# Performance work log

Hardware: AMD Instinct MI355X
Metric: run time of the kernel (lower is better)

Reference implementation:

```python
import jax, jax.numpy as jnp
import numpy as np

N = 50000   # nodes
E = 800000  # edges (avg degree 16)
D = 128     # emb_dim
K = 3       # message passing rounds


def setup_inputs() -> dict:
    key = jax.random.key(0)
    ks = jax.random.split(key, 24)
    scale = jnp.float32(0.1)  # keep k iterated MLP magnitudes sane

    def w(k, shape):
        return jax.random.normal(k, shape, dtype=jnp.float32) * scale

    inp = {
        "feat": jax.random.normal(ks[0], (N, D), dtype=jnp.float32),
        "src": jax.random.randint(ks[1], (E,), 0, N, dtype=jnp.int32),
        "dst": jax.random.randint(ks[2], (E,), 0, N, dtype=jnp.int32),
    }
    i = 3
    for name in ["nt", "fp", "fu", "bp", "bu"]:
        inp[name + "_w1"] = w(ks[i], (D, D))
        inp[name + "_b1"] = w(ks[i + 1], (D,))
        inp[name + "_w2"] = w(ks[i + 2], (D, D))
        inp[name + "_b2"] = w(ks[i + 3], (D,))
        i += 4
    return inp


def _fnn(x, w1, b1, w2, b2):
    # FNN(in,[hid],out): Linear -> ReLU -> Linear (no final activation)
    return jnp.maximum(x @ w1 + b1, 0.0) @ w2 + b2


def _aggregate(y, src, dst, pw1, pb1, pw2, pb2, uw1, ub1, uw2, ub2):
    # gather src node states -> edge MLP (+ReLU) -> scatter-sum -> node MLP (+ReLU)
    msg = jnp.maximum(_fnn(y[src], pw1, pb1, pw2, pb2), 0.0)   # [E, D]
    z = jax.ops.segment_sum(msg, dst, num_segments=N)          # [N, D]
    return jnp.maximum(_fnn(z, uw1, ub1, uw2, ub2), 0.0)       # [N, D]


def _message_pass(self_trans, src, dst, sink, params):
    y = self_trans
    for _ in range(K):
        h = _aggregate(y, src, dst, *params)
        h = h.at[sink].set(0.0)  # zero the sink node row
        y = self_trans + h
    return y


def reference(feat, src, dst,
              nt_w1, nt_b1, nt_w2, nt_b2,
              fp_w1, fp_b1, fp_w2, fp_b2,
              fu_w1, fu_b1, fu_w2, fu_b2,
              bp_w1, bp_b1, bp_w2, bp_b2,
              bu_w1, bu_b1, bu_w2, bu_b2):
    self_trans = _fnn(feat, nt_w1, nt_b1, nt_w2, nt_b2)  # [N, D]
    # forward-direction aggregator, sink = last node
    out_fpa = _message_pass(self_trans, src, dst, N - 1,
                            (fp_w1, fp_b1, fp_w2, fp_b2,
                             fu_w1, fu_b1, fu_w2, fu_b2))
    # reversed graph (dgl.reverse swaps src/dst), sink = node 0
    out_bpa = _message_pass(self_trans, dst, src, 0,
                            (bp_w1, bp_b1, bp_w2, bp_b2,
                             bu_w1, bu_b1, bu_w2, bu_b2))
    return jnp.concatenate([out_fpa, out_bpa], axis=1)  # [N, 2D]
```

## Files before the change

kernel.cpp:

```cpp
#include <hip/hip_runtime.h>

#define Nn 50000
#define Ee 800000
#define Dd 128
#define Kk 3
#define TEA 32
#define NT 256

#define LSTR 136
#define WSLOT 32768

#define NBUK 196
#define SCH 2048
#define SB ((Ee + SCH - 1) / SCH)
#define FCAP 5632

typedef short sh8 __attribute__((ext_vector_type(8)));
typedef float f32x4 __attribute__((ext_vector_type(4)));

__device__ __forceinline__ ushort bfsplit(float x, float* rem) {
  const unsigned u = __float_as_uint(x);
  *rem = x - __uint_as_float(u & 0xffff0000u);
  return (ushort)(u >> 16);
}
__device__ __forceinline__ ushort bftrunc(float x) {
  return (ushort)(__float_as_uint(x) >> 16);
}
__device__ __forceinline__ ushort f32_to_bf16_rtn(float x) {
  const unsigned u = __float_as_uint(x);
  return (ushort)((u + 0x7fffu + ((u >> 16) & 1u)) >> 16);
}

__device__ __forceinline__ void acc8(const uint4 v, float4& a0, float4& a1) {
  a0.x += __uint_as_float(v.x << 16);
  a0.y += __uint_as_float(v.x & 0xffff0000u);
  a0.z += __uint_as_float(v.y << 16);
  a0.w += __uint_as_float(v.y & 0xffff0000u);
  a1.x += __uint_as_float(v.z << 16);
  a1.y += __uint_as_float(v.z & 0xffff0000u);
  a1.z += __uint_as_float(v.w << 16);
  a1.w += __uint_as_float(v.w & 0xffff0000u);
}

#define MFMA_LAYER(WH, WL, MT)                                                 \
  {                                                                            \
    _Pragma("unroll")                                                          \
    for (int c = 0; c < 4; ++c) {                                              \
      const sh8 bh0 = *(const sh8*)((WH) + (((nt0    ) * 4 + c) * 64 + lane) * 8); \
      const sh8 bh1 = *(const sh8*)((WH) + (((nt0 + 1) * 4 + c) * 64 + lane) * 8); \
      const sh8 bl0 = *(const sh8*)((WL) + (((nt0    ) * 4 + c) * 64 + lane) * 8); \
      const sh8 bl1 = *(const sh8*)((WL) + (((nt0 + 1) * 4 + c) * 64 + lane) * 8); \
      _Pragma("unroll")                                                        \
      for (int mt = 0; mt < (MT); ++mt) {                                      \
        const int aoff = (mt * 16 + l15) * LSTR + c * 32 + q8 * 8;             \
        const sh8 ah = *(const sh8*)(Sh + aoff);                               \
        const sh8 al = *(const sh8*)(Sl + aoff);                               \
        acc[mt][0] = __builtin_amdgcn_mfma_f32_16x16x32_bf16(ah, bh0, acc[mt][0], 0, 0, 0); \
        acc[mt][1] = __builtin_amdgcn_mfma_f32_16x16x32_bf16(ah, bh1, acc[mt][1], 0, 0, 0); \
        acc[mt][0] = __builtin_amdgcn_mfma_f32_16x16x32_bf16(al, bh0, acc[mt][0], 0, 0, 0); \
        acc[mt][1] = __builtin_amdgcn_mfma_f32_16x16x32_bf16(al, bh1, acc[mt][1], 0, 0, 0); \
        acc[mt][0] = __builtin_amdgcn_mfma_f32_16x16x32_bf16(ah, bl0, acc[mt][0], 0, 0, 0); \
        acc[mt][1] = __builtin_amdgcn_mfma_f32_16x16x32_bf16(ah, bl1, acc[mt][1], 0, 0, 0); \
      }                                                                        \
    }                                                                          \
  }

#define ZERO_ACC(MT)                                             \
  {                                                              \
    _Pragma("unroll")                                            \
    for (int mt = 0; mt < (MT); ++mt)                            \
      _Pragma("unroll")                                          \
      for (int nl = 0; nl < 2; ++nl) {                           \
        acc[mt][nl][0] = 0.f; acc[mt][nl][1] = 0.f;              \
        acc[mt][nl][2] = 0.f; acc[mt][nl][3] = 0.f;              \
      }                                                          \
  }

#define HIDDEN_TO_LDS(B1ptr, MT)                                 \
  {                                                              \
    const float b1a = (B1ptr)[w32 + l15];                        \
    const float b1b = (B1ptr)[w32 + 16 + l15];                   \
    _Pragma("unroll")                                            \
    for (int mt = 0; mt < (MT); ++mt)                            \
      _Pragma("unroll")                                          \
      for (int nl = 0; nl < 2; ++nl) {                           \
        const int col = w32 + nl * 16 + l15;                     \
        const float bb = nl ? b1b : b1a;                         \
        _Pragma("unroll")                                        \
        for (int rg = 0; rg < 4; ++rg) {                         \
          const int row = mt * 16 + q8 * 4 + rg;                 \
          const float h = fmaxf(acc[mt][nl][rg] + bb, 0.f);      \
          float rm;                                              \
          const ushort hh = bfsplit(h, &rm);                     \
          const int off = row * LSTR + col;                      \
          Sh[off] = hh;                                          \
          Sl[off] = bftrunc(rm);                                 \
        }                                                        \
      }                                                          \
  }

#define STC_TO_LDS(MT)                                           \
  {                                                              \
    _Pragma("unroll")                                            \
    for (int mt = 0; mt < (MT); ++mt)                            \
      _Pragma("unroll")                                          \
      for (int nl = 0; nl < 2; ++nl) {                           \
        const int col = w32 + nl * 16 + l15;                     \
        _Pragma("unroll")                                        \
        for (int rg = 0; rg < 4; ++rg) {                         \
          const int row = mt * 16 + q8 * 4 + rg;                 \
          float rm;                                              \
          const ushort hh = bfsplit(stc[mt][nl][rg], &rm);       \
          const int off = row * LSTR + col;                      \
          Sh[off] = hh;                                          \
          Sl[off] = bftrunc(rm);                                 \
        }                                                        \
      }                                                          \
  }

#define STAGE_ROWS(Xptr)                                                       \
  {                                                                            \
    _Pragma("unroll")                                                          \
    for (int it = 0; it < (TEA * 32 / NT); ++it) {                             \
      const int i = t + NT * it;                                               \
      const int r = i >> 5;                                                    \
      const int c4 = (i & 31) << 2;                                            \
      float4 v = make_float4(0.f, 0.f, 0.f, 0.f);                              \
      if (r < nrow) v = *(const float4*)((Xptr) + (size_t)(row0 + r) * Dd + c4); \
      ushort4 hv, lv; float rm;                                                \
      hv.x = bfsplit(v.x, &rm); lv.x = bftrunc(rm);                            \
      hv.y = bfsplit(v.y, &rm); lv.y = bftrunc(rm);                            \
      hv.z = bfsplit(v.z, &rm); lv.z = bftrunc(rm);                            \
      hv.w = bfsplit(v.w, &rm); lv.w = bftrunc(rm);                            \
      *(ushort4*)(&Sh[r * LSTR + c4]) = hv;                                    \
      *(ushort4*)(&Sl[r * LSTR + c4]) = lv;                                    \
    }                                                                          \
  }

#define MFMA_PRELUDE(MT)                                         \
  const int lane = t & 63;                                       \
  const int wave = t >> 6;                                       \
  const int l15 = lane & 15;                                     \
  const int q8 = lane >> 4;                                      \
  const int w32 = wave * 32;                                     \
  const int nt0 = wave * 2;                                      \
  f32x4 acc[MT][2];

struct DirP {
  const ushort *u1, *u2, *p1, *p2;
  const float *ub1, *ub2, *pb1, *pb2;
};

__global__ __launch_bounds__(NT) void stmsg_kernel(
    const float* __restrict__ X,
    const ushort* __restrict__ Wn1, const ushort* __restrict__ Wn2,
    const float* __restrict__ Bn1, const float* __restrict__ Bn2,
    DirP pf, DirP pb,
    float* __restrict__ st, ushort* __restrict__ Mf, ushort* __restrict__ Mb)
{
  __shared__ __align__(16) ushort Sbuf[2 * TEA * LSTR];
  ushort* Sh = Sbuf;
  ushort* Sl = Sbuf + TEA * LSTR;
  const int t = threadIdx.x;
  const int row0 = blockIdx.x * TEA;
  const int rem = Nn - row0;
  const int nrow = rem < TEA ? rem : TEA;

  STAGE_ROWS(X);
  __syncthreads();
  MFMA_PRELUDE(2);

  ZERO_ACC(2);
  MFMA_LAYER(Wn1, Wn1 + 16384, 2);
  __syncthreads();
  HIDDEN_TO_LDS(Bn1, 2);
  __syncthreads();
  ZERO_ACC(2);
  MFMA_LAYER(Wn2, Wn2 + 16384, 2);

  float stc[2][2][4];
  {
    const float b2a = Bn2[w32 + l15];
    const float b2b = Bn2[w32 + 16 + l15];
    #pragma unroll
    for (int mt = 0; mt < 2; ++mt)
      #pragma unroll
      for (int nl = 0; nl < 2; ++nl) {
        const int col = w32 + nl * 16 + l15;
        const float bb = nl ? b2b : b2a;
        #pragma unroll
        for (int rg = 0; rg < 4; ++rg) {
          const int row = mt * 16 + q8 * 4 + rg;
          const float v = acc[mt][nl][rg] + bb;
          stc[mt][nl][rg] = v;
          if (row < nrow) st[(size_t)(row0 + row) * Dd + col] = v;
        }
      }
  }
  __syncthreads();

  STC_TO_LDS(2);
  __syncthreads();
  ZERO_ACC(2);
  MFMA_LAYER(pf.p1, pf.p1 + 16384, 2);
  __syncthreads();
  HIDDEN_TO_LDS(pf.pb1, 2);
  __syncthreads();
  ZERO_ACC(2);
  MFMA_LAYER(pf.p2, pf.p2 + 16384, 2);
  {
    const float b2a = pf.pb2[w32 + l15];
    const float b2b = pf.pb2[w32 + 16 + l15];
    #pragma unroll
    for (int mt = 0; mt < 2; ++mt)
      #pragma unroll
      for (int nl = 0; nl < 2; ++nl) {
        const int col = w32 + nl * 16 + l15;
        const float bb = nl ? b2b : b2a;
        #pragma unroll
        for (int rg = 0; rg < 4; ++rg) {
          const int row = mt * 16 + q8 * 4 + rg;
          if (row < nrow)
            Mf[(size_t)(row0 + row) * Dd + col] =
                f32_to_bf16_rtn(fmaxf(acc[mt][nl][rg] + bb, 0.f));
        }
      }
  }
  __syncthreads();

  STC_TO_LDS(2);
  __syncthreads();
  ZERO_ACC(2);
  MFMA_LAYER(pb.p1, pb.p1 + 16384, 2);
  __syncthreads();
  HIDDEN_TO_LDS(pb.pb1, 2);
  __syncthreads();
  ZERO_ACC(2);
  MFMA_LAYER(pb.p2, pb.p2 + 16384, 2);
  {
    const float b2a = pb.pb2[w32 + l15];
    const float b2b = pb.pb2[w32 + 16 + l15];
    #pragma unroll
    for (int mt = 0; mt < 2; ++mt)
      #pragma unroll
      for (int nl = 0; nl < 2; ++nl) {
        const int col = w32 + nl * 16 + l15;
        const float bb = nl ? b2b : b2a;
        #pragma unroll
        for (int rg = 0; rg < 4; ++rg) {
          const int row = mt * 16 + q8 * 4 + rg;
          if (row < nrow)
            Mb[(size_t)(row0 + row) * Dd + col] =
                f32_to_bf16_rtn(fmaxf(acc[mt][nl][rg] + bb, 0.f));
        }
      }
  }
}

template <int DO_MSG>
__global__ __launch_bounds__(NT) void aggupdmsg_kernel(
    const ushort* __restrict__ Min_f, const ushort* __restrict__ Min_b,
    const int* __restrict__ rp_f, const int* __restrict__ rp_b,
    const int* __restrict__ col_f, const int* __restrict__ col_b,
    const float* __restrict__ st,
    ushort* __restrict__ RMf, ushort* __restrict__ RMb,
    float* __restrict__ RYf, float* __restrict__ RYb, int rstride,
    DirP pf, DirP pb, int nhalf)
{
  __shared__ __align__(16) ushort Sbuf[2 * TEA * LSTR];
  ushort* Sh = Sbuf;
  ushort* Sl = Sbuf + TEA * LSTR;
  const int t = threadIdx.x;
  const int dir = blockIdx.x >= nhalf;
  const int row0 = (blockIdx.x - dir * nhalf) * TEA;
  const int rem = Nn - row0;
  const int nrow = rem < TEA ? rem : TEA;
  const DirP P = dir ? pb : pf;
  const ushort* Min = dir ? Min_b : Min_f;
  const int* rp = dir ? rp_b : rp_f;
  const int* col = dir ? col_b : col_f;
  ushort* RoutM = dir ? RMb : RMf;
  float* RoutY = dir ? RYb : RYf;
  const int sink = dir ? 0 : (Nn - 1);

  {
    const int nr = t >> 3;
    const int o8 = t & 7;
    float4 za[4];
    #pragma unroll
    for (int i = 0; i < 4; ++i) za[i] = make_float4(0.f, 0.f, 0.f, 0.f);
    if (nr < nrow) {
      const int gnode = row0 + nr;
      int e = rp[gnode];
      const int ee = rp[gnode + 1];
      const ushort* Mo = Min + o8 * 16;
      for (; e + 3 < ee; e += 4) {
        const int c0 = col[e];
        const int c1 = col[e + 1];
        const int c2 = col[e + 2];
        const int c3 = col[e + 3];
        const ushort* r0 = Mo + (size_t)c0 * Dd;
        const ushort* r1 = Mo + (size_t)c1 * Dd;
        const ushort* r2 = Mo + (size_t)c2 * Dd;
        const ushort* r3 = Mo + (size_t)c3 * Dd;
        uint4 a0 = *(const uint4*)(r0), b0 = *(const uint4*)(r0 + 8);
        uint4 a1 = *(const uint4*)(r1), b1 = *(const uint4*)(r1 + 8);
        uint4 a2 = *(const uint4*)(r2), b2 = *(const uint4*)(r2 + 8);
        uint4 a3 = *(const uint4*)(r3), b3 = *(const uint4*)(r3 + 8);
        acc8(a0, za[0], za[1]); acc8(b0, za[2], za[3]);
        acc8(a1, za[0], za[1]); acc8(b1, za[2], za[3]);
        acc8(a2, za[0], za[1]); acc8(b2, za[2], za[3]);
        acc8(a3, za[0], za[1]); acc8(b3, za[2], za[3]);
      }
      for (; e < ee; ++e) {
        const ushort* r0 = Mo + (size_t)col[e] * Dd;
        acc8(*(const uint4*)(r0), za[0], za[1]);
        acc8(*(const uint4*)(r0 + 8), za[2], za[3]);
      }
    }
    #pragma unroll
    for (int k = 0; k < 4; ++k) {
      ushort4 hv, lv; float rm;
      hv.x = bfsplit(za[k].x, &rm); lv.x = bftrunc(rm);
      hv.y = bfsplit(za[k].y, &rm); lv.y = bftrunc(rm);
      hv.z = bfsplit(za[k].z, &rm); lv.z = bftrunc(rm);
      hv.w = bfsplit(za[k].w, &rm); lv.w = bftrunc(rm);
      const int c4 = o8 * 16 + k * 4;
      *(ushort4*)(&Sh[nr * LSTR + c4]) = hv;
      *(ushort4*)(&Sl[nr * LSTR + c4]) = lv;
    }
  }
  __syncthreads();

  MFMA_PRELUDE(2);

  ZERO_ACC(2);
  MFMA_LAYER(P.u1, P.u1 + 16384, 2);
  __syncthreads();
  HIDDEN_TO_LDS(P.ub1, 2);
  __syncthreads();
  ZERO_ACC(2);
  MFMA_LAYER(P.u2, P.u2 + 16384, 2);

  {
    const float b2a = P.ub2[w32 + l15];
    const float b2b = P.ub2[w32 + 16 + l15];
    if (DO_MSG) __syncthreads();
    #pragma unroll
    for (int mt = 0; mt < 2; ++mt)
      #pragma unroll
      for (int nl = 0; nl < 2; ++nl) {
        const int col = w32 + nl * 16 + l15;
        const float bb = nl ? b2b : b2a;
        #pragma unroll
        for (int rg = 0; rg < 4; ++rg) {
          const int row = mt * 16 + q8 * 4 + rg;
          float v = 0.f;
          if (row < nrow) {
            const int gr = row0 + row;
            v = fmaxf(acc[mt][nl][rg] + bb, 0.f);
            if (gr == sink) v = 0.f;
            v += st[(size_t)gr * Dd + col];
          }
          if (DO_MSG) {
            float rm;
            const ushort hh = bfsplit(v, &rm);
            const int off = row * LSTR + col;
            Sh[off] = hh;
            Sl[off] = bftrunc(rm);
          } else if (row < nrow) {
            RoutY[(size_t)(row0 + row) * rstride + col] = v;
          }
        }
      }
  }

  if (DO_MSG) {
    __syncthreads();
    ZERO_ACC(2);
    MFMA_LAYER(P.p1, P.p1 + 16384, 2);
    __syncthreads();
    HIDDEN_TO_LDS(P.pb1, 2);
    __syncthreads();
    ZERO_ACC(2);
    MFMA_LAYER(P.p2, P.p2 + 16384, 2);

    const float b2a = P.pb2[w32 + l15];
    const float b2b = P.pb2[w32 + 16 + l15];
    #pragma unroll
    for (int mt = 0; mt < 2; ++mt)
      #pragma unroll
      for (int nl = 0; nl < 2; ++nl) {
        const int col = w32 + nl * 16 + l15;
        const float bb = nl ? b2b : b2a;
        #pragma unroll
        for (int rg = 0; rg < 4; ++rg) {
          const int row = mt * 16 + q8 * 4 + rg;
          if (row < nrow)
            RoutM[(size_t)(row0 + row) * Dd + col] =
                f32_to_bf16_rtn(fmaxf(acc[mt][nl][rg] + bb, 0.f));
        }
      }
  }
}

struct WPtrs { const float* w[10]; };

__global__ __launch_bounds__(256) void csr_count(
    const int* __restrict__ src, const int* __restrict__ dst,
    int* __restrict__ bcnt)
{
  const int dirv = blockIdx.y;
  const int* key = dirv ? src : dst;
  __shared__ int h[NBUK];
  const int t = threadIdx.x;
  if (t < NBUK) h[t] = 0;
  __syncthreads();
  const int e0 = blockIdx.x * SCH;
  #pragma unroll
  for (int i = 0; i < SCH / 256; ++i) {
    const int e = e0 + i * 256 + t;
    if (e < Ee) atomicAdd(&h[key[e] >> 8], 1);
  }
  __syncthreads();
  if (t < NBUK && h[t] > 0) atomicAdd(&bcnt[dirv * 256 + t], h[t]);
}

__global__ __launch_bounds__(256) void csr_scan_pack(
    const int* __restrict__ bcnt, int* __restrict__ bbase,
    int* __restrict__ bcur, int* __restrict__ rp,
    WPtrs P, ushort* __restrict__ out)
{
  const int t = threadIdx.x;
  if (blockIdx.x == 0) {
    __shared__ int s[256];
    for (int y = 0; y < 2; ++y) {
      const int v = (t < NBUK) ? bcnt[y * 256 + t] : 0;
      s[t] = v;
      __syncthreads();
      for (int off = 1; off < 256; off <<= 1) {
        int x = s[t];
        if (t >= off) x += s[t - off];
        __syncthreads();
        s[t] = x;
        __syncthreads();
      }
      const int excl = s[t] - v;
      if (t < NBUK) { bbase[y * 257 + t] = excl; bcur[y * 256 + t] = excl; }
      if (t == NBUK - 1) bbase[y * 257 + NBUK] = s[t];
      if (t == 0) rp[y * (Nn + 1) + Nn] = Ee;
      __syncthreads();
    }
  } else {
    const int work = (blockIdx.x - 1) * 256 + t;
    const int mat = work >> 14;
    const int id = work & 16383;
    const int j = id & 7;
    const int lane = (id >> 3) & 63;
    const int ch = (id >> 9) & 3;
    const int nt = id >> 11;
    const int k = ch * 32 + (lane >> 4) * 8 + j;
    const int n = nt * 16 + (lane & 15);
    const float x = P.w[mat][k * Dd + n];
    float rm;
    const ushort h = bfsplit(x, &rm);
    out[(size_t)mat * WSLOT + id] = h;
    out[(size_t)mat * WSLOT + 16384 + id] = bftrunc(rm);
  }
}

__global__ __launch_bounds__(256) void csr_scatter(
    const int* __restrict__ src, const int* __restrict__ dst,
    int* __restrict__ bcur, uint* __restrict__ pairs)
{
  const int dirv = blockIdx.y;
  const int* key = dirv ? src : dst;
  const int* val = dirv ? dst : src;
  __shared__ int lh[NBUK], gb[NBUK], lc[NBUK];
  const int t = threadIdx.x;
  if (t < NBUK) { lh[t] = 0; lc[t] = 0; }
  __syncthreads();
  const int e0 = blockIdx.x * SCH;
  int ks[SCH / 256], vs[SCH / 256];
  #pragma unroll
  for (int i = 0; i < SCH / 256; ++i) {
    const int e = e0 + i * 256 + t;
    ks[i] = (e < Ee) ? key[e] : -1;
    vs[i] = (e < Ee) ? val[e] : 0;
    if (ks[i] >= 0) atomicAdd(&lh[ks[i] >> 8], 1);
  }
  __syncthreads();
  if (t < NBUK && lh[t] > 0) gb[t] = atomicAdd(&bcur[dirv * 256 + t], lh[t]);
  __syncthreads();
  uint* pd = pairs + (size_t)dirv * Ee;
  #pragma unroll
  for (int i = 0; i < SCH / 256; ++i) {
    if (ks[i] >= 0) {
      const int b = ks[i] >> 8;
      const int r = atomicAdd(&lc[b], 1);
      pd[gb[b] + r] = ((uint)ks[i] << 16) | (uint)vs[i];
    }
  }
}

__global__ __launch_bounds__(256) void csr_final(
    const uint* __restrict__ pairs, const int* __restrict__ bbase,
    int* __restrict__ rp, int* __restrict__ col_f, int* __restrict__ col_b)
{
  const int dirv = blockIdx.y;
  const int b = blockIdx.x;
  const int base = bbase[dirv * 257 + b];
  const int cnt = bbase[dirv * 257 + b + 1] - base;
  const uint* pd = pairs + (size_t)dirv * Ee + base;
  int* colo = dirv ? col_b : col_f;
  __shared__ int h[256];
  __shared__ int s[256];
  __shared__ uint pr[FCAP];
  const int t = threadIdx.x;
  h[t] = 0;
  __syncthreads();
  const bool fits = (cnt <= FCAP);
  if (fits) {
    for (int i = t; i < cnt; i += 256) {
      const uint p = pd[i];
      pr[i] = p;
      atomicAdd(&h[(p >> 16) & 255], 1);
    }
  } else {
    for (int i = t; i < cnt; i += 256) atomicAdd(&h[(pd[i] >> 16) & 255], 1);
  }
  __syncthreads();
  const int v = h[t];
  s[t] = v;
  __syncthreads();
  for (int off = 1; off < 256; off <<= 1) {
    int x = s[t];
    if (t >= off) x += s[t - off];
    __syncthreads();
    s[t] = x;
    __syncthreads();
  }
  const int excl = s[t] - v;
  const int node = b * 256 + t;
  if (node < Nn) rp[dirv * (Nn + 1) + node] = base + excl;
  h[t] = excl;
  __syncthreads();
  if (fits) {
    for (int band = 0; band < 8; ++band) {
      for (int i = t; i < cnt; i += 256) {
        const uint p = pr[i];
        const int vv = (int)(p & 0xffffu);
        if ((vv >> 13) == band) {
          const int k = (p >> 16) & 255;
          const int r = atomicAdd(&h[k], 1);
          colo[base + r] = vv;
        }
      }
      __syncthreads();
    }
  } else {
    for (int i = t; i < cnt; i += 256) {
      const uint p = pd[i];
      const int k = (p >> 16) & 255;
      const int r = atomicAdd(&h[k], 1);
      colo[base + r] = (int)(p & 0xffffu);
    }
  }
}

extern "C" void kernel_launch(void* const* d_in, const int* in_sizes, int n_in,
                              void* d_out, int out_size, void* d_ws, size_t ws_size,
                              hipStream_t stream)
{
  const float* feat = (const float*)d_in[0];
  const int*   src  = (const int*)d_in[1];
  const int*   dst  = (const int*)d_in[2];

  const float* W[5][4];
  for (int p = 0; p < 5; ++p)
    for (int q = 0; q < 4; ++q)
      W[p][q] = (const float*)d_in[3 + p * 4 + q];

  float* st = (float*)d_ws;
  ushort* Mp_f = (ushort*)(st + (size_t)Nn * Dd);
  ushort* Mp_b = Mp_f + (size_t)Nn * Dd;
  ushort* Mq_f = Mp_b + (size_t)Nn * Dd;
  ushort* Mq_b = Mq_f + (size_t)Nn * Dd;
  int* ip       = (int*)(Mq_b + (size_t)Nn * Dd);
  int* rp_f     = ip;                 ip += Nn + 1;
  int* rp_b     = ip;                 ip += Nn + 1;
  int* col_f    = ip;                 ip += Ee;
  int* col_b    = ip;                 ip += Ee;
  int* bcnt     = ip;                 ip += 2 * 256;
  int* bbase    = ip;                 ip += 2 * 257;
  int* bcur     = ip;                 ip += 2 * 256;
  ushort* Wp = (ushort*)(((uintptr_t)ip + 63) & ~(uintptr_t)63);
  float* out = (float*)d_out;

  uint* pairs = (uint*)Mq_f;

  const int aggBlocks  = (Nn + TEA - 1) / TEA;
  const int dualBlocks = 2 * aggBlocks;

  WPtrs wpk;
  for (int p = 0; p < 5; ++p) { wpk.w[2 * p] = W[p][0]; wpk.w[2 * p + 1] = W[p][2]; }

  hipMemsetAsync(bcnt, 0, 2 * 256 * sizeof(int), stream);
  csr_count<<<dim3(SB, 2), 256, 0, stream>>>(src, dst, bcnt);
  csr_scan_pack<<<641, 256, 0, stream>>>(bcnt, bbase, bcur, rp_f, wpk, Wp);
  csr_scatter<<<dim3(SB, 2), 256, 0, stream>>>(src, dst, bcur, pairs);
  csr_final<<<dim3(NBUK, 2), 256, 0, stream>>>(pairs, bbase, rp_f, col_f, col_b);

  #define WS(m) (Wp + (size_t)(m) * WSLOT)
  DirP Pf = { WS(4), WS(5), WS(2), WS(3), W[2][1], W[2][3], W[1][1], W[1][3] };
  DirP Pb = { WS(8), WS(9), WS(6), WS(7), W[4][1], W[4][3], W[3][1], W[3][3] };

  stmsg_kernel<<<aggBlocks, NT, 0, stream>>>(
      feat, WS(0), WS(1), W[0][1], W[0][3], Pf, Pb, st, Mp_f, Mp_b);

  aggupdmsg_kernel<1><<<dualBlocks, NT, 0, stream>>>(
      Mp_f, Mp_b, rp_f, rp_b, col_f, col_b, st,
      Mq_f, Mq_b, nullptr, nullptr, 0, Pf, Pb, aggBlocks);

  aggupdmsg_kernel<1><<<dualBlocks, NT, 0, stream>>>(
      Mq_f, Mq_b, rp_f, rp_b, col_f, col_b, st,
      Mp_f, Mp_b, nullptr, nullptr, 0, Pf, Pb, aggBlocks);

  aggupdmsg_kernel<0><<<dualBlocks, NT, 0, stream>>>(
      Mp_f, Mp_b, rp_f, rp_b, col_f, col_b, st,
      nullptr, nullptr, out, out + Dd, 2 * Dd, Pf, Pb, aggBlocks);

  #undef WS
}
```

Baseline: 525.2 us.

## Fuse CSR scatter blocks into self-transform/message kernel grid

Merges the edge scatter pass and the initial node/message MLP kernel into one launch. The first blocks of the grid do the bucket scatter and the rest do the MLP rows. This removes a kernel launch and its serialization, so the memory-bound scatter can overlap with the compute-bound MLP. The MLP blocks now share the grid with scatter blocks that have a different resource profile.

```diff
diff --git a/kernel.cpp b/kernel.cpp
--- a/kernel.cpp
+++ b/kernel.cpp
@@ -151,18 +151,122 @@
   const float *ub1, *ub2, *pb1, *pb2;
 };
 
-__global__ __launch_bounds__(NT) void stmsg_kernel(
+struct WPtrs { const float* w[10]; };
+
+__global__ __launch_bounds__(256) void csr_count(
+    const int* __restrict__ src, const int* __restrict__ dst,
+    int* __restrict__ bcnt)
+{
+  const int dirv = blockIdx.y;
+  const int* key = dirv ? src : dst;
+  __shared__ int h[NBUK];
+  const int t = threadIdx.x;
+  if (t < NBUK) h[t] = 0;
+  __syncthreads();
+  const int e0 = blockIdx.x * SCH;
+  #pragma unroll
+  for (int i = 0; i < SCH / 256; ++i) {
+    const int e = e0 + i * 256 + t;
+    if (e < Ee) atomicAdd(&h[key[e] >> 8], 1);
+  }
+  __syncthreads();
+  if (t < NBUK && h[t] > 0) atomicAdd(&bcnt[dirv * 256 + t], h[t]);
+}
+
+__global__ __launch_bounds__(256) void csr_scan_pack(
+    const int* __restrict__ bcnt, int* __restrict__ bbase,
+    int* __restrict__ bcur, int* __restrict__ rp,
+    WPtrs P, ushort* __restrict__ out)
+{
+  const int t = threadIdx.x;
+  if (blockIdx.x == 0) {
+    __shared__ int s[256];
+    for (int y = 0; y < 2; ++y) {
+      const int v = (t < NBUK) ? bcnt[y * 256 + t] : 0;
+      s[t] = v;
+      __syncthreads();
+      for (int off = 1; off < 256; off <<= 1) {
+        int x = s[t];
+        if (t >= off) x += s[t - off];
+        __syncthreads();
+        s[t] = x;
+        __syncthreads();
+      }
+      const int excl = s[t] - v;
+      if (t < NBUK) { bbase[y * 257 + t] = excl; bcur[y * 256 + t] = excl; }
+      if (t == NBUK - 1) bbase[y * 257 + NBUK] = s[t];
+      if (t == 0) rp[y * (Nn + 1) + Nn] = Ee;
+      __syncthreads();
+    }
+  } else {
+    const int work = (blockIdx.x - 1) * 256 + t;
+    const int mat = work >> 14;
+    const int id = work & 16383;
+    const int j = id & 7;
+    const int lane = (id >> 3) & 63;
+    const int ch = (id >> 9) & 3;
+    const int nt = id >> 11;
+    const int k = ch * 32 + (lane >> 4) * 8 + j;
+    const int n = nt * 16 + (lane & 15);
+    const float x = P.w[mat][k * Dd + n];
+    float rm;
+    const ushort h = bfsplit(x, &rm);
+    out[(size_t)mat * WSLOT + id] = h;
+    out[(size_t)mat * WSLOT + 16384 + id] = bftrunc(rm);
+  }
+}
+
+__global__ __launch_bounds__(NT) void scatter_stmsg_kernel(
+    const int* __restrict__ src, const int* __restrict__ dst,
+    int* __restrict__ bcur, uint* __restrict__ pairs,
     const float* __restrict__ X,
     const ushort* __restrict__ Wn1, const ushort* __restrict__ Wn2,
     const float* __restrict__ Bn1, const float* __restrict__ Bn2,
     DirP pf, DirP pb,
-    float* __restrict__ st, ushort* __restrict__ Mf, ushort* __restrict__ Mb)
+    float* __restrict__ st, ushort* __restrict__ Mf, ushort* __restrict__ Mb,
+    int nScatter)
 {
   __shared__ __align__(16) ushort Sbuf[2 * TEA * LSTR];
+  const int t = threadIdx.x;
+
+  if ((int)blockIdx.x < nScatter) {
+    int* lh = (int*)Sbuf;
+    int* gb = lh + 256;
+    int* lc = gb + 256;
+    const int dirv = (int)blockIdx.x >= SB;
+    const int sb = blockIdx.x - dirv * SB;
+    const int* key = dirv ? src : dst;
+    const int* val = dirv ? dst : src;
+    if (t < NBUK) { lh[t] = 0; lc[t] = 0; }
+    __syncthreads();
+    const int e0 = sb * SCH;
+    int ks[SCH / 256], vs[SCH / 256];
+    #pragma unroll
+    for (int i = 0; i < SCH / 256; ++i) {
+      const int e = e0 + i * 256 + t;
+      ks[i] = (e < Ee) ? key[e] : -1;
+      vs[i] = (e < Ee) ? val[e] : 0;
+      if (ks[i] >= 0) atomicAdd(&lh[ks[i] >> 8], 1);
+    }
+    __syncthreads();
+    if (t < NBUK && lh[t] > 0) gb[t] = atomicAdd(&bcur[dirv * 256 + t], lh[t]);
+    __syncthreads();
+    uint* pd = pairs + (size_t)dirv * Ee;
+    #pragma unroll
+    for (int i = 0; i < SCH / 256; ++i) {
+      if (ks[i] >= 0) {
+        const int b = ks[i] >> 8;
+        const int r = atomicAdd(&lc[b], 1);
+        pd[gb[b] + r] = ((uint)ks[i] << 16) | (uint)vs[i];
+      }
+    }
+    return;
+  }
+
   ushort* Sh = Sbuf;
   ushort* Sl = Sbuf + TEA * LSTR;
-  const int t = threadIdx.x;
-  const int row0 = blockIdx.x * TEA;
+  const int bid = blockIdx.x - nScatter;
+  const int row0 = bid * TEA;
   const int rem = Nn - row0;
   const int nrow = rem < TEA ? rem : TEA;
 
@@ -254,6 +358,71 @@
                 f32_to_bf16_rtn(fmaxf(acc[mt][nl][rg] + bb, 0.f));
         }
       }
+  }
+}
+
+__global__ __launch_bounds__(256) void csr_final(
+    const uint* __restrict__ pairs, const int* __restrict__ bbase,
+    int* __restrict__ rp, int* __restrict__ col_f, int* __restrict__ col_b)
+{
+  const int dirv = blockIdx.y;
+  const int b = blockIdx.x;
+  const int base = bbase[dirv * 257 + b];
+  const int cnt = bbase[dirv * 257 + b + 1] - base;
+  const uint* pd = pairs + (size_t)dirv * Ee + base;
+  int* colo = dirv ? col_b : col_f;
+  __shared__ int h[256];
+  __shared__ int s[256];
+  __shared__ uint pr[FCAP];
+  const int t = threadIdx.x;
+  h[t] = 0;
+  __syncthreads();
+  const bool fits = (cnt <= FCAP);
+  if (fits) {
+    for (int i = t; i < cnt; i += 256) {
+      const uint p = pd[i];
+      pr[i] = p;
+      atomicAdd(&h[(p >> 16) & 255], 1);
+    }
+  } else {
+    for (int i = t; i < cnt; i += 256) atomicAdd(&h[(pd[i] >> 16) & 255], 1);
+  }
+  __syncthreads();
+  const int v = h[t];
+  s[t] = v;
+  __syncthreads();
+  for (int off = 1; off < 256; off <<= 1) {
+    int x = s[t];
+    if (t >= off) x += s[t - off];
+    __syncthreads();
+    s[t] = x;
+    __syncthreads();
+  }
+  const int excl = s[t] - v;
+  const int node = b * 256 + t;
+  if (node < Nn) rp[dirv * (Nn + 1) + node] = base + excl;
+  h[t] = excl;
+  __syncthreads();
+  if (fits) {
+    for (int band = 0; band < 8; ++band) {
+      for (int i = t; i < cnt; i += 256) {
+        const uint p = pr[i];
+        const int vv = (int)(p & 0xffffu);
+        if ((vv >> 13) == band) {
+          const int k = (p >> 16) & 255;
+          const int r = atomicAdd(&h[k], 1);
+          colo[base + r] = vv;
+        }
+      }
+      __syncthreads();
+    }
+  } else {
+    for (int i = t; i < cnt; i += 256) {
+      const uint p = pd[i];
+      const int k = (p >> 16) & 255;
+      const int r = atomicAdd(&h[k], 1);
+      colo[base + r] = (int)(p & 0xffffu);
+    }
   }
 }
 
@@ -404,170 +573,6 @@
   }
 }
 
-struct WPtrs { const float* w[10]; };
-
-__global__ __launch_bounds__(256) void csr_count(
-    const int* __restrict__ src, const int* __restrict__ dst,
-    int* __restrict__ bcnt)
-{
-  const int dirv = blockIdx.y;
-  const int* key = dirv ? src : dst;
-  __shared__ int h[NBUK];
-  const int t = threadIdx.x;
-  if (t < NBUK) h[t] = 0;
-  __syncthreads();
-  const int e0 = blockIdx.x * SCH;
-  #pragma unroll
-  for (int i = 0; i < SCH / 256; ++i) {
-    const int e = e0 + i * 256 + t;
-    if (e < Ee) atomicAdd(&h[key[e] >> 8], 1);
-  }
-  __syncthreads();
-  if (t < NBUK && h[t] > 0) atomicAdd(&bcnt[dirv * 256 + t], h[t]);
-}
-
-__global__ __launch_bounds__(256) void csr_scan_pack(
-    const int* __restrict__ bcnt, int* __restrict__ bbase,
-    int* __restrict__ bcur, int* __restrict__ rp,
-    WPtrs P, ushort* __restrict__ out)
-{
-  const int t = threadIdx.x;
-  if (blockIdx.x == 0) {
-    __shared__ int s[256];
-    for (int y = 0; y < 2; ++y) {
-      const int v = (t < NBUK) ? bcnt[y * 256 + t] : 0;
-      s[t] = v;
-      __syncthreads();
-      for (int off = 1; off < 256; off <<= 1) {
-        int x = s[t];
-        if (t >= off) x += s[t - off];
-        __syncthreads();
-        s[t] = x;
-        __syncthreads();
-      }
-      const int excl = s[t] - v;
-      if (t < NBUK) { bbase[y * 257 + t] = excl; bcur[y * 256 + t] = excl; }
-      if (t == NBUK - 1) bbase[y * 257 + NBUK] = s[t];
-      if (t == 0) rp[y * (Nn + 1) + Nn] = Ee;
-      __syncthreads();
-    }
-  } else {
-    const int work = (blockIdx.x - 1) * 256 + t;
-    const int mat = work >> 14;
-    const int id = work & 16383;
-    const int j = id & 7;
-    const int lane = (id >> 3) & 63;
-    const int ch = (id >> 9) & 3;
-    const int nt = id >> 11;
-    const int k = ch * 32 + (lane >> 4) * 8 + j;
-    const int n = nt * 16 + (lane & 15);
-    const float x = P.w[mat][k * Dd + n];
-    float rm;
-    const ushort h = bfsplit(x, &rm);
-    out[(size_t)mat * WSLOT + id] = h;
-    out[(size_t)mat * WSLOT + 16384 + id] = bftrunc(rm);
-  }
-}
-
-__global__ __launch_bounds__(256) void csr_scatter(
-    const int* __restrict__ src, const int* __restrict__ dst,
-    int* __restrict__ bcur, uint* __restrict__ pairs)
-{
-  const int dirv = blockIdx.y;
-  const int* key = dirv ? src : dst;
-  const int* val = dirv ? dst : src;
-  __shared__ int lh[NBUK], gb[NBUK], lc[NBUK];
-  const int t = threadIdx.x;
-  if (t < NBUK) { lh[t] = 0; lc[t] = 0; }
-  __syncthreads();
-  const int e0 = blockIdx.x * SCH;
-  int ks[SCH / 256], vs[SCH / 256];
-  #pragma unroll
-  for (int i = 0; i < SCH / 256; ++i) {
-    const int e = e0 + i * 256 + t;
-    ks[i] = (e < Ee) ? key[e] : -1;
-    vs[i] = (e < Ee) ? val[e] : 0;
-    if (ks[i] >= 0) atomicAdd(&lh[ks[i] >> 8], 1);
-  }
-  __syncthreads();
-  if (t < NBUK && lh[t] > 0) gb[t] = atomicAdd(&bcur[dirv * 256 + t], lh[t]);
-  __syncthreads();
-  uint* pd = pairs + (size_t)dirv * Ee;
-  #pragma unroll
-  for (int i = 0; i < SCH / 256; ++i) {
-    if (ks[i] >= 0) {
-      const int b = ks[i] >> 8;
-      const int r = atomicAdd(&lc[b], 1);
-      pd[gb[b] + r] = ((uint)ks[i] << 16) | (uint)vs[i];
-    }
-  }
-}
-
-__global__ __launch_bounds__(256) void csr_final(
-    const uint* __restrict__ pairs, const int* __restrict__ bbase,
-    int* __restrict__ rp, int* __restrict__ col_f, int* __restrict__ col_b)
-{
-  const int dirv = blockIdx.y;
-  const int b = blockIdx.x;
-  const int base = bbase[dirv * 257 + b];
-  const int cnt = bbase[dirv * 257 + b + 1] - base;
-  const uint* pd = pairs + (size_t)dirv * Ee + base;
-  int* colo = dirv ? col_b : col_f;
-  __shared__ int h[256];
-  __shared__ int s[256];
-  __shared__ uint pr[FCAP];
-  const int t = threadIdx.x;
-  h[t] = 0;
-  __syncthreads();
-  const bool fits = (cnt <= FCAP);
-  if (fits) {
-    for (int i = t; i < cnt; i += 256) {
-      const uint p = pd[i];
-      pr[i] = p;
-      atomicAdd(&h[(p >> 16) & 255], 1);
-    }
-  } else {
-    for (int i = t; i < cnt; i += 256) atomicAdd(&h[(pd[i] >> 16) & 255], 1);
-  }
-  __syncthreads();
-  const int v = h[t];
-  s[t] = v;
-  __syncthreads();
-  for (int off = 1; off < 256; off <<= 1) {
-    int x = s[t];
-    if (t >= off) x += s[t - off];
-    __syncthreads();
-    s[t] = x;
-    __syncthreads();
-  }
-  const int excl = s[t] - v;
-  const int node = b * 256 + t;
-  if (node < Nn) rp[dirv * (Nn + 1) + node] = base + excl;
-  h[t] = excl;
-  __syncthreads();
-  if (fits) {
-    for (int band = 0; band < 8; ++band) {
-      for (int i = t; i < cnt; i += 256) {
-        const uint p = pr[i];
-        const int vv = (int)(p & 0xffffu);
-        if ((vv >> 13) == band) {
-          const int k = (p >> 16) & 255;
-          const int r = atomicAdd(&h[k], 1);
-          colo[base + r] = vv;
-        }
-      }
-      __syncthreads();
-    }
-  } else {
-    for (int i = t; i < cnt; i += 256) {
-      const uint p = pd[i];
-      const int k = (p >> 16) & 255;
-      const int r = atomicAdd(&h[k], 1);
-      colo[base + r] = (int)(p & 0xffffu);
-    }
-  }
-}
-
 extern "C" void kernel_launch(void* const* d_in, const int* in_sizes, int n_in,
                               void* d_out, int out_size, void* d_ws, size_t ws_size,
                               hipStream_t stream)
@@ -601,22 +606,22 @@
 
   const int aggBlocks  = (Nn + TEA - 1) / TEA;
   const int dualBlocks = 2 * aggBlocks;
+  const int nScatter   = 2 * SB;
 
   WPtrs wpk;
   for (int p = 0; p < 5; ++p) { wpk.w[2 * p] = W[p][0]; wpk.w[2 * p + 1] = W[p][2]; }
+
+  #define WS(m) (Wp + (size_t)(m) * WSLOT)
+  DirP Pf = { WS(4), WS(5), WS(2), WS(3), W[2][1], W[2][3], W[1][1], W[1][3] };
+  DirP Pb = { WS(8), WS(9), WS(6), WS(7), W[4][1], W[4][3], W[3][1], W[3][3] };
 
   hipMemsetAsync(bcnt, 0, 2 * 256 * sizeof(int), stream);
   csr_count<<<dim3(SB, 2), 256, 0, stream>>>(src, dst, bcnt);
   csr_scan_pack<<<641, 256, 0, stream>>>(bcnt, bbase, bcur, rp_f, wpk, Wp);
-  csr_scatter<<<dim3(SB, 2), 256, 0, stream>>>(src, dst, bcur, pairs);
+  scatter_stmsg_kernel<<<nScatter + aggBlocks, NT, 0, stream>>>(
+      src, dst, bcur, pairs, feat, WS(0), WS(1), W[0][1], W[0][3],
+      Pf, Pb, st, Mp_f, Mp_b, nScatter);
   csr_final<<<dim3(NBUK, 2), 256, 0, stream>>>(pairs, bbase, rp_f, col_f, col_b);
-
-  #define WS(m) (Wp + (size_t)(m) * WSLOT)
-  DirP Pf = { WS(4), WS(5), WS(2), WS(3), W[2][1], W[2][3], W[1][1], W[1][3] };
-  DirP Pb = { WS(8), WS(9), WS(6), WS(7), W[4][1], W[4][3], W[3][1], W[3][3] };
-
-  stmsg_kernel<<<aggBlocks, NT, 0, stream>>>(
-      feat, WS(0), WS(1), W[0][1], W[0][3], Pf, Pb, st, Mp_f, Mp_b);
 
   aggupdmsg_kernel<1><<<dualBlocks, NT, 0, stream>>>(
       Mp_f, Mp_b, rp_f, rp_b, col_f, col_b, st,
```

Result: no change. 523.4 us (-0.3%).
